# Kernel tuning notes

Measured on AMD Instinct MI355X. Metric: run time of the kernel, lower is better.

The kernel has to match this reference:

```python
import jax, jax.numpy as jnp
import numpy as np

EPS = 1e-5
NEG_SLOPE = 0.1
K = 3
KK = K * K
PAD = 1


def conv3x3(x, w, b):
    # x: [B,C,H,W], w: [O,C,3,3], zero padding 1, stride 1
    y = jax.lax.conv_general_dilated(x, w, (1, 1), [(PAD, PAD), (PAD, PAD)],
                                     dimension_numbers=('NCHW', 'OIHW', 'NCHW'))
    return y + b[None, :, None, None]


def deform_conv(x, off_w, off_b, mod_w, mod_b, w):
    # modulated deformable conv v2 (torchvision.ops.deform_conv2d semantics)
    B, C, H, W = x.shape
    offset = conv3x3(x, off_w, off_b)                      # [B,2*KK,H,W]
    mask = 2.0 * jax.nn.sigmoid(conv3x3(x, mod_w, mod_b))  # [B,KK,H,W]
    off = offset.reshape(B, KK, 2, H, W)                   # (dy,dx) per kernel pos

    ky = (jnp.arange(KK) // K).astype(x.dtype)  # kernel row of tap k
    kx = (jnp.arange(KK) % K).astype(x.dtype)   # kernel col of tap k
    hh = jnp.arange(H, dtype=x.dtype)
    ww = jnp.arange(W, dtype=x.dtype)

    # sampling positions: [B,KK,H,W]
    py = hh[None, None, :, None] - PAD + ky[None, :, None, None] + off[:, :, 0]
    px = ww[None, None, None, :] - PAD + kx[None, :, None, None] + off[:, :, 1]

    y0 = jnp.floor(py)
    x0 = jnp.floor(px)
    dy = py - y0
    dx = px - x0

    x_flat = x.reshape(B, C, H * W)

    def gather(yi, xi):
        # zero-padded bilinear corner gather -> [B,C,KK,H,W]
        valid = (yi >= 0) & (yi < H) & (xi >= 0) & (xi < W)
        yc = jnp.clip(yi, 0, H - 1).astype(jnp.int32)
        xc = jnp.clip(xi, 0, W - 1).astype(jnp.int32)
        idx = (yc * W + xc).reshape(B, 1, KK * H * W)
        g = jnp.take_along_axis(x_flat, jnp.broadcast_to(idx, (B, C, KK * H * W)), axis=2)
        return g.reshape(B, C, KK, H, W) * valid[:, None].astype(x.dtype)

    wy = dy[:, None]  # [B,1,KK,H,W]
    wx = dx[:, None]
    samp = (gather(y0, x0) * (1 - wy) * (1 - wx)
            + gather(y0, x0 + 1) * (1 - wy) * wx
            + gather(y0 + 1, x0) * wy * (1 - wx)
            + gather(y0 + 1, x0 + 1) * wy * wx)
    samp = samp * mask[:, None]
    # main conv as contraction over (C, KK)
    return jnp.einsum('bckhw,ock->bohw', samp, w.reshape(w.shape[0], C, KK))


def batch_norm(x, gamma, beta):
    # training-mode BatchNorm2d: stats over (B,H,W), biased variance
    mean = jnp.mean(x, axis=(0, 2, 3), keepdims=True)
    var = jnp.mean(jnp.square(x - mean), axis=(0, 2, 3), keepdims=True)
    xn = (x - mean) * jax.lax.rsqrt(var + EPS)
    return xn * gamma[None, :, None, None] + beta[None, :, None, None]


def leaky_relu(x):
    return jnp.where(x >= 0, x, NEG_SLOPE * x)


def setup_inputs() -> dict:
    key = jax.random.key(0)
    ks = jax.random.split(key, 12)
    B, C, H, W = 4, 96, 128, 128
    s = 1.0 / np.sqrt(C * KK)
    d = {
        'x': jax.random.normal(ks[0], (B, C, H, W), jnp.float32),
        'd1_off_w': jax.random.normal(ks[1], (2 * KK, C, K, K), jnp.float32) * s,
        'd1_off_b': jnp.zeros((2 * KK,), jnp.float32),
        'd1_mod_w': jax.random.normal(ks[2], (KK, C, K, K), jnp.float32) * s,
        'd1_mod_b': jnp.zeros((KK,), jnp.float32),
        'd1_w': jax.random.normal(ks[3], (C, C, K, K), jnp.float32) * s,
        'd2_off_w': jax.random.normal(ks[4], (2 * KK, C, K, K), jnp.float32) * s,
        'd2_off_b': jnp.zeros((2 * KK,), jnp.float32),
        'd2_mod_w': jax.random.normal(ks[5], (KK, C, K, K), jnp.float32) * s,
        'd2_mod_b': jnp.zeros((KK,), jnp.float32),
        'd2_w': jax.random.normal(ks[6], (C, C, K, K), jnp.float32) * s,
        'bn_g': jnp.ones((C,), jnp.float32),
        'bn_b': jnp.zeros((C,), jnp.float32),
    }
    return d


def reference(x, d1_off_w, d1_off_b, d1_mod_w, d1_mod_b, d1_w,
              d2_off_w, d2_off_b, d2_mod_w, d2_mod_b, d2_w, bn_g, bn_b):
    h = deform_conv(x, d1_off_w, d1_off_b, d1_mod_w, d1_mod_b, d1_w)
    h = leaky_relu(batch_norm(h, bn_g, bn_b))
    h = deform_conv(h, d2_off_w, d2_off_b, d2_mod_w, d2_mod_b, d2_w)
    h = batch_norm(h, bn_g, bn_b)  # same shared BN module (shared params)
    return x + h
```

## Files before the change

### kernel.cpp

```cpp
#include <hip/hip_runtime.h>
#include <math.h>

#define NB 4
#define NC 96
#define NH 128
#define NW 128
#define HWSZ (NH * NW)
#define NK 9
#define AUXC 27
#define CKK (NC * NK)
#define WC_ELEMS (32 * CKK)
#define WBS_STEP 4096
#define WBS_SHORTS (27 * WBS_STEP)
#define PIXB (NC * 2)
#define ZOFF ((unsigned int)(NB * HWSZ * PIXB))

typedef __attribute__((ext_vector_type(8))) short bf16x8;
typedef __attribute__((ext_vector_type(4))) float f32x4;

__device__ __forceinline__ unsigned int bf16r(float f) {
    unsigned int u = __float_as_uint(f);
    u += 0x7fffu + ((u >> 16) & 1u);
    return u >> 16;
}
__device__ __forceinline__ float uaf(unsigned int u) { return __uint_as_float(u); }

__device__ __forceinline__ unsigned int cvtpk(float lo, float hi) {
    unsigned int u;
    asm("v_cvt_pk_bf16_f32 %0, %1, %2" : "=v"(u) : "v"(lo), "v"(hi));
    return u;
}

__device__ __forceinline__ void gload_lds16(const void* g, void* l) {
    __builtin_amdgcn_global_load_lds(
        (const __attribute__((address_space(1))) void*)g,
        (__attribute__((address_space(3))) void*)l, 16, 0, 0);
}

__global__ __launch_bounds__(256) void prep_weights_kernel(
    const float* __restrict__ offw, const float* __restrict__ modw,
    const float* __restrict__ w,
    unsigned short* __restrict__ wc16, unsigned short* __restrict__ wbs)
{
    int idx = blockIdx.x * 256 + threadIdx.x;
    if (idx < WC_ELEMS) {
        int oc  = idx / CKK;
        int rem = idx - oc * CKK;
        int tap = rem / NC;
        int c   = rem - tap * NC;
        float v = 0.f;
        if (oc < 18)      v = offw[oc * CKK + c * NK + tap];
        else if (oc < 27) v = modw[(oc - 18) * CKK + c * NK + tap];
        wc16[idx] = (unsigned short)bf16r(v);
    }
    int j = idx - WC_ELEMS;
    if (j >= 0 && j < WBS_SHORTS) {
        int st = j >> 12;
        int r  = j & 4095;
        int oc = r / 40;
        int k2 = r - oc * 40;
        unsigned short v = 0;
        if (oc < NC && k2 < 32) {
            int tap = st / 3;
            int c   = (st - 3 * tap) * 32 + k2;
            v = (unsigned short)bf16r(w[oc * CKK + c * NK + tap]);
        }
        wbs[j] = v;
    }
}

__global__ __launch_bounds__(256) void nhwc_kernel(
    const float* __restrict__ in, unsigned short* __restrict__ o)
{
    __shared__ unsigned short tile[64][98];
    int t = threadIdx.x;
    int blk = blockIdx.x;
    int b  = blk >> 8;
    int p0 = (blk & 255) * 64;

    if (blk == 0 && t < NC) o[(size_t)NB * HWSZ * NC + t] = 0;

    const float* ib = in + (size_t)b * NC * HWSZ + p0;
#pragma unroll
    for (int r = 0; r < 12; ++r) {
        int e = (r * 256 + t) * 2;
        int c = e >> 6, px = e & 63;
        float2 v = *(const float2*)(ib + c * HWSZ + px);
        tile[px][c]     = (unsigned short)bf16r(v.x);
        tile[px + 1][c] = (unsigned short)bf16r(v.y);
    }
    __syncthreads();

    unsigned short* ob = o + ((size_t)b * HWSZ + p0) * NC;
#pragma unroll
    for (int r = 0; r < 12; ++r) {
        int e = (r * 256 + t) * 2;
        int px = e / 96, c = e - px * 96;
        ushort2 u;
        u.x = tile[px][c];
        u.y = tile[px][c + 1];
        *(ushort2*)(ob + e) = u;
    }
}

__global__ __launch_bounds__(256) void nhwcbn_kernel(
    const float* __restrict__ in, const float* __restrict__ sc,
    unsigned short* __restrict__ o)
{
    __shared__ unsigned short tile[64][98];
    int t = threadIdx.x;
    int blk = blockIdx.x;
    int b  = blk >> 8;
    int p0 = (blk & 255) * 64;

    const float* ib = in + (size_t)b * NC * HWSZ + p0;
#pragma unroll
    for (int r = 0; r < 12; ++r) {
        int e = (r * 256 + t) * 2;
        int c = e >> 6, px = e & 63;
        float scale = sc[c], shift = sc[NC + c];
        float2 v = *(const float2*)(ib + c * HWSZ + px);
        float ox = fmaf(scale, v.x, shift); ox = ox >= 0.f ? ox : 0.1f * ox;
        float oy = fmaf(scale, v.y, shift); oy = oy >= 0.f ? oy : 0.1f * oy;
        tile[px][c]     = (unsigned short)bf16r(ox);
        tile[px + 1][c] = (unsigned short)bf16r(oy);
    }
    __syncthreads();

    unsigned short* ob = o + ((size_t)b * HWSZ + p0) * NC;
#pragma unroll
    for (int r = 0; r < 12; ++r) {
        int e = (r * 256 + t) * 2;
        int px = e / 96, c = e - px * 96;
        ushort2 u;
        u.x = tile[px][c];
        u.y = tile[px][c + 1];
        *(ushort2*)(ob + e) = u;
    }
}

__global__ __launch_bounds__(512, 4) void conv27_mfma_kernel(
    const unsigned short* __restrict__ xhwc,
    const unsigned short* __restrict__ wc16,
    const float* __restrict__ offb, const float* __restrict__ modb,
    float* __restrict__ aux)
{
    __shared__ unsigned int sOff[NK][66];
    __shared__ float sRed[4][8][64];

    int t = threadIdx.x;
    int bid = blockIdx.x;
    int work = ((bid & 7) << 7) | (bid >> 3);
    int base = work * 64;
    int b = base >> 14;
    int rem0 = base & (HWSZ - 1);
    int y = rem0 >> 7;
    int x0 = rem0 & (NW - 1);

    for (int e = t; e < 576; e += 512) {
        int px = e & 63, k = e >> 6;
        int ky = k / 3, kx = k - 3 * (k / 3);
        int yy = y + ky - 1, xx = x0 + px + kx - 1;
        bool v = (yy >= 0) && (yy < NH) && (xx >= 0) && (xx < NW);
        sOff[k][px] = v ? (unsigned int)(((b << 14) + yy * NW + xx) * PIXB)
                        : ZOFF;
    }
    __syncthreads();

    f32x4 acc[2];
    acc[0] = (f32x4){0.f, 0.f, 0.f, 0.f};
    acc[1] = (f32x4){0.f, 0.f, 0.f, 0.f};

    const int lane15   = t & 15;
    const int g        = (t >> 4) & 3;
    const int wv       = t >> 6;
    const int nt       = wv & 3;
    const int ks       = wv >> 2;
    const int px_local = (nt << 4) | lane15;
    const int g8       = g << 3;
    const int l64      = t & 63;

    const int stbeg = ks ? 14 : 0;
    const int stend = ks ? 27 : 14;

    const char* pB = (const char*)xhwc;

    int st = stbeg;
    int tap = st / 3;
    int c2  = ((st - 3 * tap) * 32 + g8) * 2;
    bf16x8 bfr = *(const bf16x8*)(pB + sOff[tap][px_local] + c2);
    bf16x8 a0  = *(const bf16x8*)(wc16 + (size_t)lane15 * CKK + st * 32 + g8);
    bf16x8 a1  = *(const bf16x8*)(wc16 + (size_t)(16 + lane15) * CKK + st * 32 + g8);

    for (; st < stend; ++st) {
        int stn  = (st + 1 < stend) ? st + 1 : stbeg;
        int tapn = stn / 3;
        int c2n  = ((stn - 3 * tapn) * 32 + g8) * 2;
        bf16x8 bn  = *(const bf16x8*)(pB + sOff[tapn][px_local] + c2n);
        bf16x8 a0n = *(const bf16x8*)(wc16 + (size_t)lane15 * CKK + stn * 32 + g8);
        bf16x8 a1n = *(const bf16x8*)(wc16 + (size_t)(16 + lane15) * CKK + stn * 32 + g8);

        acc[0] = __builtin_amdgcn_mfma_f32_16x16x32_bf16(a0, bfr, acc[0], 0, 0, 0);
        acc[1] = __builtin_amdgcn_mfma_f32_16x16x32_bf16(a1, bfr, acc[1], 0, 0, 0);
        bfr = bn; a0 = a0n; a1 = a1n;
    }

    if (ks == 1) {
#pragma unroll
        for (int i = 0; i < 2; ++i)
#pragma unroll
            for (int r = 0; r < 4; ++r)
                sRed[nt][i * 4 + r][l64] = acc[i][r];
    }
    __syncthreads();
    if (ks == 0) {
        float* ap = aux + (size_t)b * AUXC * HWSZ + y * NW + x0 + px_local;
#pragma unroll
        for (int i = 0; i < 2; ++i) {
#pragma unroll
            for (int r = 0; r < 4; ++r) {
                int oc = i * 16 + g * 4 + r;
                float v = acc[i][r] + sRed[nt][i * 4 + r][l64];
                if (oc < 18) {
                    ap[oc * HWSZ] = v + offb[oc];
                } else if (oc < AUXC) {
                    float z = v + modb[oc - 18];
                    ap[oc * HWSZ] = 2.f / (1.f + __expf(-z));
                }
            }
        }
    }
}

__global__ __launch_bounds__(512, 4) void deform_mfma_kernel(
    const unsigned short* __restrict__ xhwc,
    const float* __restrict__ aux,
    const unsigned short* __restrict__ wbs,
    float* __restrict__ out)
{
    __shared__ uint4 sA[NK][NW];
    __shared__ uint2 sW[NK][NW];
    __shared__ unsigned short ws[2][WBS_STEP];

    int t = threadIdx.x;
    int bid = blockIdx.x;
    int work = ((bid & 7) << 6) | (bid >> 3);
    int b = work >> 7;
    int y = work & 127;

    const float* auxb = aux + (size_t)b * AUXC * HWSZ;

    for (int e = t; e < NK * NW; e += 512) {
        int px = e & 127;
        int k  = e >> 7;
        int idx = y * NW + px;
        float offy = auxb[(2 * k) * HWSZ + idx];
        float offx = auxb[(2 * k + 1) * HWSZ + idx];
        float m    = auxb[(18 + k) * HWSZ + idx];
        int ky = k / 3, kx = k - 3 * (k / 3);
        float py  = (float)(y - 1 + ky) + offy;
        float pxf = (float)(px - 1 + kx) + offx;
        float y0f = floorf(py), x0f = floorf(pxf);
        float dy = py - y0f, dx = pxf - x0f;
        int iy0 = (int)y0f, ix0 = (int)x0f;
        int iy1 = iy0 + 1,  ix1 = ix0 + 1;

        bool vy0 = (iy0 >= 0) && (iy0 < NH);
        bool vy1 = (iy1 >= 0) && (iy1 < NH);
        bool vx0 = (ix0 >= 0) && (ix0 < NW);
        bool vx1 = (ix1 >= 0) && (ix1 < NW);
        int cy0 = min(max(iy0, 0), NH - 1);
        int cy1 = min(max(iy1, 0), NH - 1);
        int cx0 = min(max(ix0, 0), NW - 1);
        int cx1 = min(max(ix1, 0), NW - 1);

        float g00 = (1.f - dy) * (1.f - dx) * m; if (!(vy0 && vx0)) g00 = 0.f;
        float g01 = (1.f - dy) * dx * m;         if (!(vy0 && vx1)) g01 = 0.f;
        float g10 = dy * (1.f - dx) * m;         if (!(vy1 && vx0)) g10 = 0.f;
        float g11 = dy * dx * m;                 if (!(vy1 && vx1)) g11 = 0.f;

        uint4 ua;
        ua.x = (unsigned int)(cy0 * NW + cx0) * PIXB;
        ua.y = (unsigned int)(cy0 * NW + cx1) * PIXB;
        ua.z = (unsigned int)(cy1 * NW + cx0) * PIXB;
        ua.w = (unsigned int)(cy1 * NW + cx1) * PIXB;
        uint2 uw;
        uw.x = bf16r(g00) | (bf16r(g01) << 16);
        uw.y = bf16r(g10) | (bf16r(g11) << 16);
        sA[k][px] = ua;
        sW[k][px] = uw;
    }

    gload_lds16((const char*)wbs + (size_t)t * 16, (char*)&ws[0][0] + t * 16);
    __syncthreads();

    f32x4 acc[6];
#pragma unroll
    for (int i = 0; i < 6; ++i) acc[i] = (f32x4){0.f, 0.f, 0.f, 0.f};

    const int lane15   = t & 15;
    const int g        = (t >> 4) & 3;
    const int wv       = t >> 6;
    const int px_local = (wv << 4) | lane15;
    const int g8       = g << 3;

    const char* pB = (const char*)(xhwc + (size_t)b * HWSZ * NC);

    uint4 ga = sA[0][px_local];
    uint2 gw = sW[0][px_local];
    bf16x8 v0 = *(const bf16x8*)(pB + ga.x + (g8 << 1));
    bf16x8 v1 = *(const bf16x8*)(pB + ga.y + (g8 << 1));
    bf16x8 v2 = *(const bf16x8*)(pB + ga.z + (g8 << 1));
    bf16x8 v3 = *(const bf16x8*)(pB + ga.w + (g8 << 1));

    int buf = 0;
    for (int st = 0; st < 27; ++st) {
        bool more = (st + 1 < 27);
        uint4 gaN; uint2 gwN;
        bf16x8 n0, n1, n2, n3;
        if (more) {
            gload_lds16((const char*)wbs + (size_t)(st + 1) * (WBS_STEP * 2) + t * 16,
                        (char*)&ws[buf ^ 1][0] + t * 16);
            int kn  = (st + 1) / 3;
            int c2n = ((st + 1 - 3 * kn) * 32 + g8) * 2;
            gaN = sA[kn][px_local];
            gwN = sW[kn][px_local];
            n0 = *(const bf16x8*)(pB + gaN.x + c2n);
            n1 = *(const bf16x8*)(pB + gaN.y + c2n);
            n2 = *(const bf16x8*)(pB + gaN.z + c2n);
            n3 = *(const bf16x8*)(pB + gaN.w + c2n);
        }

        bf16x8 afr[6];
#pragma unroll
        for (int i = 0; i < 6; ++i)
            afr[i] = *(const bf16x8*)(&ws[buf][(i * 16 + lane15) * 40 + g8]);

        float w00 = uaf(gw.x << 16), w01 = uaf(gw.x & 0xffff0000u);
        float w10 = uaf(gw.y << 16), w11 = uaf(gw.y & 0xffff0000u);
        float s[8];
#pragma unroll
        for (int j = 0; j < 8; ++j) {
            float f0 = uaf((unsigned int)(unsigned short)v0[j] << 16);
            float f1 = uaf((unsigned int)(unsigned short)v1[j] << 16);
            float f2 = uaf((unsigned int)(unsigned short)v2[j] << 16);
            float f3 = uaf((unsigned int)(unsigned short)v3[j] << 16);
            float sv = f0 * w00;
            sv = fmaf(f1, w01, sv);
            sv = fmaf(f2, w10, sv);
            sv = fmaf(f3, w11, sv);
            s[j] = sv;
        }
        union { bf16x8 h; unsigned int u[4]; } uu;
#pragma unroll
        for (int jj = 0; jj < 4; ++jj)
            uu.u[jj] = cvtpk(s[2 * jj], s[2 * jj + 1]);
        bf16x8 bfr = uu.h;

#pragma unroll
        for (int i = 0; i < 6; ++i)
            acc[i] = __builtin_amdgcn_mfma_f32_16x16x32_bf16(afr[i], bfr, acc[i], 0, 0, 0);

        if (more) {
            __syncthreads();
            ga = gaN; gw = gwN; v0 = n0; v1 = n1; v2 = n2; v3 = n3;
            buf ^= 1;
        }
    }

    float* ob = out + (size_t)b * NC * HWSZ + y * NW + px_local;
#pragma unroll
    for (int i = 0; i < 6; ++i) {
        int row0 = i * 16 + g * 4;
#pragma unroll
        for (int r = 0; r < 4; ++r)
            ob[(row0 + r) * HWSZ] = acc[i][r];
    }
}

__global__ __launch_bounds__(256) void bnstats_kernel(
    const float* __restrict__ h, float* __restrict__ part)
{
    int bc = blockIdx.x;
    const float4* p = (const float4*)(h + (size_t)bc * HWSZ);
    float s = 0.f, s2 = 0.f;
    for (int i = threadIdx.x; i < HWSZ / 4; i += 256) {
        float4 v = p[i];
        s  += v.x + v.y + v.z + v.w;
        s2 += v.x * v.x + v.y * v.y + v.z * v.z + v.w * v.w;
    }
#pragma unroll
    for (int o = 32; o > 0; o >>= 1) {
        s  += __shfl_down(s, o);
        s2 += __shfl_down(s2, o);
    }
    __shared__ float red[8];
    int wv = threadIdx.x >> 6, ln = threadIdx.x & 63;
    if (ln == 0) { red[wv] = s; red[4 + wv] = s2; }
    __syncthreads();
    if (threadIdx.x == 0) {
        part[bc]            = red[0] + red[1] + red[2] + red[3];
        part[NB * NC + bc]  = red[4] + red[5] + red[6] + red[7];
    }
}

__global__ __launch_bounds__(128) void bnfinalize_kernel(
    const float* __restrict__ part, const float* __restrict__ g,
    const float* __restrict__ bt, float* __restrict__ sc)
{
    int c = threadIdx.x;
    if (c >= NC) return;
    float s = 0.f, s2 = 0.f;
#pragma unroll
    for (int b = 0; b < NB; ++b) {
        s  += part[b * NC + c];
        s2 += part[NB * NC + b * NC + c];
    }
    const float inv_n = 1.f / (float)(NB * HWSZ);
    float mean = s * inv_n;
    float var  = s2 * inv_n - mean * mean;
    float scale = g[c] * rsqrtf(var + 1e-5f);
    sc[c] = scale;
    sc[NC + c] = bt[c] - mean * scale;
}

__global__ __launch_bounds__(256) void final_kernel(
    float* __restrict__ out, const float* __restrict__ x,
    const float* __restrict__ sc)
{
    const int n4 = NB * NC * HWSZ / 4;
    for (int i = blockIdx.x * 256 + threadIdx.x; i < n4; i += gridDim.x * 256) {
        int c = (i >> 12) % NC;
        float scale = sc[c], shift = sc[NC + c];
        float4 v = ((const float4*)out)[i];
        float4 xv = ((const float4*)x)[i];
        float4 o;
        o.x = xv.x + fmaf(scale, v.x, shift);
        o.y = xv.y + fmaf(scale, v.y, shift);
        o.z = xv.z + fmaf(scale, v.z, shift);
        o.w = xv.w + fmaf(scale, v.w, shift);
        ((float4*)out)[i] = o;
    }
}

extern "C" void kernel_launch(void* const* d_in, const int* in_sizes, int n_in,
                              void* d_out, int out_size, void* d_ws, size_t ws_size,
                              hipStream_t stream)
{
    const float* x        = (const float*)d_in[0];
    const float* d1_off_w = (const float*)d_in[1];
    const float* d1_off_b = (const float*)d_in[2];
    const float* d1_mod_w = (const float*)d_in[3];
    const float* d1_mod_b = (const float*)d_in[4];
    const float* d1_w     = (const float*)d_in[5];
    const float* d2_off_w = (const float*)d_in[6];
    const float* d2_off_b = (const float*)d_in[7];
    const float* d2_mod_w = (const float*)d_in[8];
    const float* d2_mod_b = (const float*)d_in[9];
    const float* d2_w     = (const float*)d_in[10];
    const float* bn_g     = (const float*)d_in[11];
    const float* bn_b     = (const float*)d_in[12];
    float* out = (float*)d_out;

    const size_t nImg = (size_t)NB * NC * HWSZ;
    float* h1   = (float*)d_ws;
    float* aux  = h1   + nImg;
    unsigned short* wc16 = (unsigned short*)(aux + (size_t)NB * AUXC * HWSZ);
    unsigned short* wbs  = wc16 + WC_ELEMS;
    float* sc   = (float*)(wbs + WBS_SHORTS);
    float* part = sc + 2 * NC;
    unsigned short* xhwc = (unsigned short*)(part + 2 * NB * NC);

    const int npix = NB * HWSZ;
    const int prep_blocks = (WC_ELEMS + WBS_SHORTS + 255) / 256;

    prep_weights_kernel<<<prep_blocks, 256, 0, stream>>>(d1_off_w, d1_mod_w, d1_w, wc16, wbs);
    nhwc_kernel<<<npix / 64, 256, 0, stream>>>(x, xhwc);
    conv27_mfma_kernel<<<npix / 64, 512, 0, stream>>>(xhwc, wc16, d1_off_b, d1_mod_b, aux);
    deform_mfma_kernel<<<NB * NH, 512, 0, stream>>>(xhwc, aux, wbs, h1);
    bnstats_kernel<<<NB * NC, 256, 0, stream>>>(h1, part);
    bnfinalize_kernel<<<1, 128, 0, stream>>>(part, bn_g, bn_b, sc);

    prep_weights_kernel<<<prep_blocks, 256, 0, stream>>>(d2_off_w, d2_mod_w, d2_w, wc16, wbs);
    nhwcbn_kernel<<<npix / 64, 256, 0, stream>>>(h1, sc, xhwc);
    conv27_mfma_kernel<<<npix / 64, 512, 0, stream>>>(xhwc, wc16, d2_off_b, d2_mod_b, aux);
    deform_mfma_kernel<<<NB * NH, 512, 0, stream>>>(xhwc, aux, wbs, out);
    bnstats_kernel<<<NB * NC, 256, 0, stream>>>(out, part);
    bnfinalize_kernel<<<1, 128, 0, stream>>>(part, bn_g, bn_b, sc);
    final_kernel<<<2048, 256, 0, stream>>>(out, x, sc);
}
```

Baseline: 182.0 us.

## Retile deform conv to 64-pixel blocks with deeper weight pipelining and packed indices

The deformable conv kernel now handles 64 pixels per 256-thread block instead of a 128-pixel row per 512-thread block, giving twice as many smaller blocks. Weight slices drop their 40-short padded row stride for an unpadded 32 stride, and four LDS buffers are used. The main loop is unrolled by two, prefetching two weight stages at a time and issuing the next sample's gathers before computing the current one, so there is one barrier per two stages. Corner pixel indices are packed as 16-bit pairs to halve LDS index storage. The unpadded stride may add LDS bank conflicts on the A-fragment reads.

```diff
diff --git a/kernel.cpp b/kernel.cpp
--- a/kernel.cpp
+++ b/kernel.cpp
@@ -10,7 +10,7 @@
 #define AUXC 27
 #define CKK (NC * NK)
 #define WC_ELEMS (32 * CKK)
-#define WBS_STEP 4096
+#define WBS_STEP 3072
 #define WBS_SHORTS (27 * WBS_STEP)
 #define PIXB (NC * 2)
 #define ZOFF ((unsigned int)(NB * HWSZ * PIXB))
@@ -55,17 +55,13 @@
     }
     int j = idx - WC_ELEMS;
     if (j >= 0 && j < WBS_SHORTS) {
-        int st = j >> 12;
-        int r  = j & 4095;
-        int oc = r / 40;
-        int k2 = r - oc * 40;
-        unsigned short v = 0;
-        if (oc < NC && k2 < 32) {
-            int tap = st / 3;
-            int c   = (st - 3 * tap) * 32 + k2;
-            v = (unsigned short)bf16r(w[oc * CKK + c * NK + tap]);
-        }
-        wbs[j] = v;
+        int st = j / WBS_STEP;
+        int r  = j - st * WBS_STEP;
+        int oc = r >> 5;
+        int k2 = r & 31;
+        int tap = st / 3;
+        int c   = (st - 3 * tap) * 32 + k2;
+        wbs[j] = (unsigned short)bf16r(w[oc * CKK + c * NK + tap]);
     }
 }
 
@@ -232,34 +228,40 @@
     }
 }
 
-__global__ __launch_bounds__(512, 4) void deform_mfma_kernel(
+struct Smp { uint2 gw; bf16x8 v0, v1, v2, v3; };
+
+__global__ __launch_bounds__(256, 4) void deform_mfma_kernel(
     const unsigned short* __restrict__ xhwc,
     const float* __restrict__ aux,
     const unsigned short* __restrict__ wbs,
     float* __restrict__ out)
 {
-    __shared__ uint4 sA[NK][NW];
-    __shared__ uint2 sW[NK][NW];
-    __shared__ unsigned short ws[2][WBS_STEP];
+    __shared__ uint2 sA[NK][64];
+    __shared__ uint2 sW[NK][64];
+    __shared__ unsigned short ws[4][WBS_STEP];
 
     int t = threadIdx.x;
     int bid = blockIdx.x;
-    int work = ((bid & 7) << 6) | (bid >> 3);
-    int b = work >> 7;
-    int y = work & 127;
+    int work = ((bid & 7) << 7) | (bid >> 3);
+    int base = work * 64;
+    int b = base >> 14;
+    int rem0 = base & (HWSZ - 1);
+    int y = rem0 >> 7;
+    int x0 = rem0 & (NW - 1);
 
     const float* auxb = aux + (size_t)b * AUXC * HWSZ;
 
-    for (int e = t; e < NK * NW; e += 512) {
-        int px = e & 127;
-        int k  = e >> 7;
-        int idx = y * NW + px;
+    for (int e = t; e < 576; e += 256) {
+        int px = e & 63;
+        int k  = e >> 6;
+        int xcol = x0 + px;
+        int idx = y * NW + xcol;
         float offy = auxb[(2 * k) * HWSZ + idx];
         float offx = auxb[(2 * k + 1) * HWSZ + idx];
         float m    = auxb[(18 + k) * HWSZ + idx];
         int ky = k / 3, kx = k - 3 * (k / 3);
         float py  = (float)(y - 1 + ky) + offy;
-        float pxf = (float)(px - 1 + kx) + offx;
+        float pxf = (float)(xcol - 1 + kx) + offx;
         float y0f = floorf(py), x0f = floorf(pxf);
         float dy = py - y0f, dx = pxf - x0f;
         int iy0 = (int)y0f, ix0 = (int)x0f;
@@ -279,11 +281,9 @@
         float g10 = dy * (1.f - dx) * m;         if (!(vy1 && vx0)) g10 = 0.f;
         float g11 = dy * dx * m;                 if (!(vy1 && vx1)) g11 = 0.f;
 
-        uint4 ua;
-        ua.x = (unsigned int)(cy0 * NW + cx0) * PIXB;
-        ua.y = (unsigned int)(cy0 * NW + cx1) * PIXB;
-        ua.z = (unsigned int)(cy1 * NW + cx0) * PIXB;
-        ua.w = (unsigned int)(cy1 * NW + cx1) * PIXB;
+        uint2 ua;
+        ua.x = (unsigned int)(cy0 * NW + cx0) | ((unsigned int)(cy0 * NW + cx1) << 16);
+        ua.y = (unsigned int)(cy1 * NW + cx0) | ((unsigned int)(cy1 * NW + cx1) << 16);
         uint2 uw;
         uw.x = bf16r(g00) | (bf16r(g01) << 16);
         uw.y = bf16r(g10) | (bf16r(g11) << 16);
@@ -291,13 +291,6 @@
         sW[k][px] = uw;
     }
 
-    gload_lds16((const char*)wbs + (size_t)t * 16, (char*)&ws[0][0] + t * 16);
-    __syncthreads();
-
-    f32x4 acc[6];
-#pragma unroll
-    for (int i = 0; i < 6; ++i) acc[i] = (f32x4){0.f, 0.f, 0.f, 0.f};
-
     const int lane15   = t & 15;
     const int g        = (t >> 4) & 3;
     const int wv       = t >> 6;
@@ -306,45 +299,49 @@
 
     const char* pB = (const char*)(xhwc + (size_t)b * HWSZ * NC);
 
-    uint4 ga = sA[0][px_local];
-    uint2 gw = sW[0][px_local];
-    bf16x8 v0 = *(const bf16x8*)(pB + ga.x + (g8 << 1));
-    bf16x8 v1 = *(const bf16x8*)(pB + ga.y + (g8 << 1));
-    bf16x8 v2 = *(const bf16x8*)(pB + ga.z + (g8 << 1));
-    bf16x8 v3 = *(const bf16x8*)(pB + ga.w + (g8 << 1));
-
-    int buf = 0;
-    for (int st = 0; st < 27; ++st) {
-        bool more = (st + 1 < 27);
-        uint4 gaN; uint2 gwN;
-        bf16x8 n0, n1, n2, n3;
-        if (more) {
-            gload_lds16((const char*)wbs + (size_t)(st + 1) * (WBS_STEP * 2) + t * 16,
-                        (char*)&ws[buf ^ 1][0] + t * 16);
-            int kn  = (st + 1) / 3;
-            int c2n = ((st + 1 - 3 * kn) * 32 + g8) * 2;
-            gaN = sA[kn][px_local];
-            gwN = sW[kn][px_local];
-            n0 = *(const bf16x8*)(pB + gaN.x + c2n);
-            n1 = *(const bf16x8*)(pB + gaN.y + c2n);
-            n2 = *(const bf16x8*)(pB + gaN.z + c2n);
-            n3 = *(const bf16x8*)(pB + gaN.w + c2n);
-        }
-
+    auto stage = [&](int s) {
+        const char* gp = (const char*)wbs + (size_t)s * (WBS_STEP * 2);
+        char* lp = (char*)&ws[s & 3][0];
+        gload_lds16(gp + t * 16, lp + t * 16);
+        if (t < 128)
+            gload_lds16(gp + 4096 + t * 16, lp + 4096 + t * 16);
+    };
+
+    auto loadSmp = [&](int st) -> Smp {
+        int tap = st / 3;
+        int c2  = ((st - 3 * tap) * 32 + g8) * 2;
+        uint2 ga = sA[tap][px_local];
+        Smp s;
+        s.gw = sW[tap][px_local];
+        unsigned a0 = (ga.x & 0xffffu) * PIXB + c2;
+        unsigned a1 = (ga.x >> 16) * PIXB + c2;
+        unsigned a2 = (ga.y & 0xffffu) * PIXB + c2;
+        unsigned a3 = (ga.y >> 16) * PIXB + c2;
+        s.v0 = *(const bf16x8*)(pB + a0);
+        s.v1 = *(const bf16x8*)(pB + a1);
+        s.v2 = *(const bf16x8*)(pB + a2);
+        s.v3 = *(const bf16x8*)(pB + a3);
+        return s;
+    };
+
+    f32x4 acc[6];
+#pragma unroll
+    for (int i = 0; i < 6; ++i) acc[i] = (f32x4){0.f, 0.f, 0.f, 0.f};
+
+    auto compute = [&](const Smp& sm, int buf) {
         bf16x8 afr[6];
 #pragma unroll
         for (int i = 0; i < 6; ++i)
-            afr[i] = *(const bf16x8*)(&ws[buf][(i * 16 + lane15) * 40 + g8]);
-
-        float w00 = uaf(gw.x << 16), w01 = uaf(gw.x & 0xffff0000u);
-        float w10 = uaf(gw.y << 16), w11 = uaf(gw.y & 0xffff0000u);
+            afr[i] = *(const bf16x8*)(&ws[buf][(i * 16 + lane15) * 32 + g8]);
+        float w00 = uaf(sm.gw.x << 16), w01 = uaf(sm.gw.x & 0xffff0000u);
+        float w10 = uaf(sm.gw.y << 16), w11 = uaf(sm.gw.y & 0xffff0000u);
         float s[8];
 #pragma unroll
         for (int j = 0; j < 8; ++j) {
-            float f0 = uaf((unsigned int)(unsigned short)v0[j] << 16);
-            float f1 = uaf((unsigned int)(unsigned short)v1[j] << 16);
-            float f2 = uaf((unsigned int)(unsigned short)v2[j] << 16);
-            float f3 = uaf((unsigned int)(unsigned short)v3[j] << 16);
+            float f0 = uaf((unsigned int)(unsigned short)sm.v0[j] << 16);
+            float f1 = uaf((unsigned int)(unsigned short)sm.v1[j] << 16);
+            float f2 = uaf((unsigned int)(unsigned short)sm.v2[j] << 16);
+            float f3 = uaf((unsigned int)(unsigned short)sm.v3[j] << 16);
             float sv = f0 * w00;
             sv = fmaf(f1, w01, sv);
             sv = fmaf(f2, w10, sv);
@@ -355,20 +352,29 @@
 #pragma unroll
         for (int jj = 0; jj < 4; ++jj)
             uu.u[jj] = cvtpk(s[2 * jj], s[2 * jj + 1]);
-        bf16x8 bfr = uu.h;
-
 #pragma unroll
         for (int i = 0; i < 6; ++i)
-            acc[i] = __builtin_amdgcn_mfma_f32_16x16x32_bf16(afr[i], bfr, acc[i], 0, 0, 0);
-
-        if (more) {
-            __syncthreads();
-            ga = gaN; gw = gwN; v0 = n0; v1 = n1; v2 = n2; v3 = n3;
-            buf ^= 1;
-        }
-    }
-
-    float* ob = out + (size_t)b * NC * HWSZ + y * NW + px_local;
+            acc[i] = __builtin_amdgcn_mfma_f32_16x16x32_bf16(afr[i], uu.h, acc[i], 0, 0, 0);
+    };
+
+    stage(0);
+    stage(1);
+    __syncthreads();
+
+    Smp s0 = loadSmp(0);
+    for (int st2 = 0; st2 < 26; st2 += 2) {
+        if (st2 + 2 < 27) stage(st2 + 2);
+        if (st2 + 3 < 27) stage(st2 + 3);
+        Smp s1 = loadSmp(st2 + 1);
+        compute(s0, st2 & 3);
+        Smp s2 = loadSmp(st2 + 2);
+        compute(s1, (st2 + 1) & 3);
+        __syncthreads();
+        s0 = s2;
+    }
+    compute(s0, 26 & 3);
+
+    float* ob = out + (size_t)b * NC * HWSZ + y * NW + x0 + px_local;
 #pragma unroll
     for (int i = 0; i < 6; ++i) {
         int row0 = i * 16 + g * 4;
@@ -477,14 +483,14 @@
     prep_weights_kernel<<<prep_blocks, 256, 0, stream>>>(d1_off_w, d1_mod_w, d1_w, wc16, wbs);
     nhwc_kernel<<<npix / 64, 256, 0, stream>>>(x, xhwc);
     conv27_mfma_kernel<<<npix / 64, 512, 0, stream>>>(xhwc, wc16, d1_off_b, d1_mod_b, aux);
-    deform_mfma_kernel<<<NB * NH, 512, 0, stream>>>(xhwc, aux, wbs, h1);
+    deform_mfma_kernel<<<npix / 64, 256, 0, stream>>>(xhwc, aux, wbs, h1);
     bnstats_kernel<<<NB * NC, 256, 0, stream>>>(h1, part);
     bnfinalize_kernel<<<1, 128, 0, stream>>>(part, bn_g, bn_b, sc);
 
     prep_weights_kernel<<<prep_blocks, 256, 0, stream>>>(d2_off_w, d2_mod_w, d2_w, wc16, wbs);
     nhwcbn_kernel<<<npix / 64, 256, 0, stream>>>(h1, sc, xhwc);
     conv27_mfma_kernel<<<npix / 64, 512, 0, stream>>>(xhwc, wc16, d2_off_b, d2_mod_b, aux);
-    deform_mfma_kernel<<<NB * NH, 512, 0, stream>>>(xhwc, aux, wbs, out);
+    deform_mfma_kernel<<<npix / 64, 256, 0, stream>>>(xhwc, aux, wbs, out);
     bnstats_kernel<<<NB * NC, 256, 0, stream>>>(out, part);
     bnfinalize_kernel<<<1, 128, 0, stream>>>(part, bn_g, bn_b, sc);
     final_kernel<<<2048, 256, 0, stream>>>(out, x, sc);
```

Measured after the change: 185.7 us. 2.0% more time.

## Stage offset/modulator conv weights into LDS via async double-buffered loads

Applied to the files above, without the earlier changes.

Repacks the 27-channel offset/modulator weights into per-k-step padded slabs of 32 rows by 40 shorts. The conv27 kernel now streams each slab into double-buffered shared memory with global_load_lds, replacing per-thread global reads of the A fragments. The padded row stride is meant to avoid LDS bank conflicts and cut redundant global traffic for the weights. In exchange the loop gains a __syncthreads per k-step, the kernel uses more LDS, and both K-halves must run in lockstep.

```diff
diff --git a/kernel.cpp b/kernel.cpp
--- a/kernel.cpp
+++ b/kernel.cpp
@@ -9,7 +9,8 @@
 #define NK 9
 #define AUXC 27
 #define CKK (NC * NK)
-#define WC_ELEMS (32 * CKK)
+#define WCS_STEP 1280
+#define WCS_SHORTS (27 * WCS_STEP)
 #define WBS_STEP 4096
 #define WBS_SHORTS (27 * WBS_STEP)
 #define PIXB (NC * 2)
@@ -40,20 +41,24 @@
 __global__ __launch_bounds__(256) void prep_weights_kernel(
     const float* __restrict__ offw, const float* __restrict__ modw,
     const float* __restrict__ w,
-    unsigned short* __restrict__ wc16, unsigned short* __restrict__ wbs)
+    unsigned short* __restrict__ wcs, unsigned short* __restrict__ wbs)
 {
     int idx = blockIdx.x * 256 + threadIdx.x;
-    if (idx < WC_ELEMS) {
-        int oc  = idx / CKK;
-        int rem = idx - oc * CKK;
-        int tap = rem / NC;
-        int c   = rem - tap * NC;
-        float v = 0.f;
-        if (oc < 18)      v = offw[oc * CKK + c * NK + tap];
-        else if (oc < 27) v = modw[(oc - 18) * CKK + c * NK + tap];
-        wc16[idx] = (unsigned short)bf16r(v);
-    }
-    int j = idx - WC_ELEMS;
+    if (idx < WCS_SHORTS) {
+        int st = idx / WCS_STEP;
+        int r  = idx - st * WCS_STEP;
+        int oc = r / 40;
+        int k2 = r - oc * 40;
+        unsigned short v = 0;
+        if (k2 < 32) {
+            int tap = st / 3;
+            int c   = (st - 3 * tap) * 32 + k2;
+            if (oc < 18)      v = (unsigned short)bf16r(offw[oc * CKK + c * NK + tap]);
+            else if (oc < 27) v = (unsigned short)bf16r(modw[(oc - 18) * CKK + c * NK + tap]);
+        }
+        wcs[idx] = v;
+    }
+    int j = idx - WCS_SHORTS;
     if (j >= 0 && j < WBS_SHORTS) {
         int st = j >> 12;
         int r  = j & 4095;
@@ -141,12 +146,13 @@
 
 __global__ __launch_bounds__(512, 4) void conv27_mfma_kernel(
     const unsigned short* __restrict__ xhwc,
-    const unsigned short* __restrict__ wc16,
+    const unsigned short* __restrict__ wcs,
     const float* __restrict__ offb, const float* __restrict__ modb,
     float* __restrict__ aux)
 {
     __shared__ unsigned int sOff[NK][66];
     __shared__ float sRed[4][8][64];
+    __shared__ unsigned short wr[2][2][WCS_STEP];
 
     int t = threadIdx.x;
     int bid = blockIdx.x;
@@ -157,20 +163,6 @@
     int y = rem0 >> 7;
     int x0 = rem0 & (NW - 1);
 
-    for (int e = t; e < 576; e += 512) {
-        int px = e & 63, k = e >> 6;
-        int ky = k / 3, kx = k - 3 * (k / 3);
-        int yy = y + ky - 1, xx = x0 + px + kx - 1;
-        bool v = (yy >= 0) && (yy < NH) && (xx >= 0) && (xx < NW);
-        sOff[k][px] = v ? (unsigned int)(((b << 14) + yy * NW + xx) * PIXB)
-                        : ZOFF;
-    }
-    __syncthreads();
-
-    f32x4 acc[2];
-    acc[0] = (f32x4){0.f, 0.f, 0.f, 0.f};
-    acc[1] = (f32x4){0.f, 0.f, 0.f, 0.f};
-
     const int lane15   = t & 15;
     const int g        = (t >> 4) & 3;
     const int wv       = t >> 6;
@@ -180,29 +172,56 @@
     const int g8       = g << 3;
     const int l64      = t & 63;
 
+    auto stageC = [&](int st0, int st1, int slot) {
+        if (st0 >= 0 && t < 160)
+            gload_lds16((const char*)wcs + (size_t)st0 * (WCS_STEP * 2) + t * 16,
+                        (char*)&wr[0][slot][0] + t * 16);
+        if (st1 >= 0 && t >= 256 && t < 416)
+            gload_lds16((const char*)wcs + (size_t)st1 * (WCS_STEP * 2) + (t - 256) * 16,
+                        (char*)&wr[1][slot][0] + (t - 256) * 16);
+    };
+
+    stageC(0, 14, 0);
+
+    for (int e = t; e < 576; e += 512) {
+        int px = e & 63, k = e >> 6;
+        int ky = k / 3, kx = k - 3 * (k / 3);
+        int yy = y + ky - 1, xx = x0 + px + kx - 1;
+        bool v = (yy >= 0) && (yy < NH) && (xx >= 0) && (xx < NW);
+        sOff[k][px] = v ? (unsigned int)(((b << 14) + yy * NW + xx) * PIXB)
+                        : ZOFF;
+    }
+    __syncthreads();
+
+    const char* pB = (const char*)xhwc;
+    auto loadB = [&](int st) -> bf16x8 {
+        int tap = st / 3;
+        int c2  = ((st - 3 * tap) * 32 + g8) * 2;
+        return *(const bf16x8*)(pB + sOff[tap][px_local] + c2);
+    };
+
+    f32x4 acc[2];
+    acc[0] = (f32x4){0.f, 0.f, 0.f, 0.f};
+    acc[1] = (f32x4){0.f, 0.f, 0.f, 0.f};
+
     const int stbeg = ks ? 14 : 0;
     const int stend = ks ? 27 : 14;
 
-    const char* pB = (const char*)xhwc;
-
-    int st = stbeg;
-    int tap = st / 3;
-    int c2  = ((st - 3 * tap) * 32 + g8) * 2;
-    bf16x8 bfr = *(const bf16x8*)(pB + sOff[tap][px_local] + c2);
-    bf16x8 a0  = *(const bf16x8*)(wc16 + (size_t)lane15 * CKK + st * 32 + g8);
-    bf16x8 a1  = *(const bf16x8*)(wc16 + (size_t)(16 + lane15) * CKK + st * 32 + g8);
-
-    for (; st < stend; ++st) {
-        int stn  = (st + 1 < stend) ? st + 1 : stbeg;
-        int tapn = stn / 3;
-        int c2n  = ((stn - 3 * tapn) * 32 + g8) * 2;
-        bf16x8 bn  = *(const bf16x8*)(pB + sOff[tapn][px_local] + c2n);
-        bf16x8 a0n = *(const bf16x8*)(wc16 + (size_t)lane15 * CKK + stn * 32 + g8);
-        bf16x8 a1n = *(const bf16x8*)(wc16 + (size_t)(16 + lane15) * CKK + stn * 32 + g8);
-
-        acc[0] = __builtin_amdgcn_mfma_f32_16x16x32_bf16(a0, bfr, acc[0], 0, 0, 0);
-        acc[1] = __builtin_amdgcn_mfma_f32_16x16x32_bf16(a1, bfr, acc[1], 0, 0, 0);
-        bfr = bn; a0 = a0n; a1 = a1n;
+    bf16x8 bfr = loadB(stbeg);
+
+    for (int i = 0; i < 14; ++i) {
+        int stc = stbeg + i;
+        stageC((i + 1 < 14) ? i + 1 : -1,
+               (15 + i < 27) ? 15 + i : -1, (i + 1) & 1);
+        bf16x8 bn = (stc + 1 < stend) ? loadB(stc + 1) : bfr;
+        if (stc < stend) {
+            bf16x8 a0 = *(const bf16x8*)(&wr[ks][i & 1][lane15 * 40 + g8]);
+            bf16x8 a1 = *(const bf16x8*)(&wr[ks][i & 1][(16 + lane15) * 40 + g8]);
+            acc[0] = __builtin_amdgcn_mfma_f32_16x16x32_bf16(a0, bfr, acc[0], 0, 0, 0);
+            acc[1] = __builtin_amdgcn_mfma_f32_16x16x32_bf16(a1, bfr, acc[1], 0, 0, 0);
+        }
+        __syncthreads();
+        bfr = bn;
     }
 
     if (ks == 1) {
@@ -465,25 +484,25 @@
     const size_t nImg = (size_t)NB * NC * HWSZ;
     float* h1   = (float*)d_ws;
     float* aux  = h1   + nImg;
-    unsigned short* wc16 = (unsigned short*)(aux + (size_t)NB * AUXC * HWSZ);
-    unsigned short* wbs  = wc16 + WC_ELEMS;
+    unsigned short* wcs = (unsigned short*)(aux + (size_t)NB * AUXC * HWSZ);
+    unsigned short* wbs = wcs + WCS_SHORTS;
     float* sc   = (float*)(wbs + WBS_SHORTS);
     float* part = sc + 2 * NC;
     unsigned short* xhwc = (unsigned short*)(part + 2 * NB * NC);
 
     const int npix = NB * HWSZ;
-    const int prep_blocks = (WC_ELEMS + WBS_SHORTS + 255) / 256;
-
-    prep_weights_kernel<<<prep_blocks, 256, 0, stream>>>(d1_off_w, d1_mod_w, d1_w, wc16, wbs);
+    const int prep_blocks = (WCS_SHORTS + WBS_SHORTS + 255) / 256;
+
+    prep_weights_kernel<<<prep_blocks, 256, 0, stream>>>(d1_off_w, d1_mod_w, d1_w, wcs, wbs);
     nhwc_kernel<<<npix / 64, 256, 0, stream>>>(x, xhwc);
-    conv27_mfma_kernel<<<npix / 64, 512, 0, stream>>>(xhwc, wc16, d1_off_b, d1_mod_b, aux);
+    conv27_mfma_kernel<<<npix / 64, 512, 0, stream>>>(xhwc, wcs, d1_off_b, d1_mod_b, aux);
     deform_mfma_kernel<<<NB * NH, 512, 0, stream>>>(xhwc, aux, wbs, h1);
     bnstats_kernel<<<NB * NC, 256, 0, stream>>>(h1, part);
     bnfinalize_kernel<<<1, 128, 0, stream>>>(part, bn_g, bn_b, sc);
 
-    prep_weights_kernel<<<prep_blocks, 256, 0, stream>>>(d2_off_w, d2_mod_w, d2_w, wc16, wbs);
+    prep_weights_kernel<<<prep_blocks, 256, 0, stream>>>(d2_off_w, d2_mod_w, d2_w, wcs, wbs);
     nhwcbn_kernel<<<npix / 64, 256, 0, stream>>>(h1, sc, xhwc);
-    conv27_mfma_kernel<<<npix / 64, 512, 0, stream>>>(xhwc, wc16, d2_off_b, d2_mod_b, aux);
+    conv27_mfma_kernel<<<npix / 64, 512, 0, stream>>>(xhwc, wcs, d2_off_b, d2_mod_b, aux);
     deform_mfma_kernel<<<NB * NH, 512, 0, stream>>>(xhwc, aux, wbs, out);
     bnstats_kernel<<<NB * NC, 256, 0, stream>>>(out, part);
     bnfinalize_kernel<<<1, 128, 0, stream>>>(part, bn_g, bn_b, sc);
```

New measurement: 164.4 us (median of 2 runs). -9.7%, faster.

## Fuse offset/mask conv into deformable conv kernel via shared-memory aux tile

Applied to the files above, without the earlier changes.

Merges the 27-channel offset/modulation convolution into the deformable-conv kernel. Each block computes offsets and masks for its row with MFMA and keeps them in shared memory rather than writing them to a global aux buffer and reading them back. This removes one launch per layer and the aux round trip through global memory. In exchange the conv work is no longer split across two k-halves, each wave now runs all 27 steps serially without software prefetch, and the block needs more shared memory, which may lower occupancy.

```diff
diff --git a/kernel.cpp b/kernel.cpp
--- a/kernel.cpp
+++ b/kernel.cpp
@@ -139,108 +139,17 @@
     }
 }
 
-__global__ __launch_bounds__(512, 4) void conv27_mfma_kernel(
+__global__ __launch_bounds__(512, 4) void fused_layer_kernel(
     const unsigned short* __restrict__ xhwc,
     const unsigned short* __restrict__ wc16,
+    const unsigned short* __restrict__ wbs,
     const float* __restrict__ offb, const float* __restrict__ modb,
-    float* __restrict__ aux)
-{
-    __shared__ unsigned int sOff[NK][66];
-    __shared__ float sRed[4][8][64];
-
-    int t = threadIdx.x;
-    int bid = blockIdx.x;
-    int work = ((bid & 7) << 7) | (bid >> 3);
-    int base = work * 64;
-    int b = base >> 14;
-    int rem0 = base & (HWSZ - 1);
-    int y = rem0 >> 7;
-    int x0 = rem0 & (NW - 1);
-
-    for (int e = t; e < 576; e += 512) {
-        int px = e & 63, k = e >> 6;
-        int ky = k / 3, kx = k - 3 * (k / 3);
-        int yy = y + ky - 1, xx = x0 + px + kx - 1;
-        bool v = (yy >= 0) && (yy < NH) && (xx >= 0) && (xx < NW);
-        sOff[k][px] = v ? (unsigned int)(((b << 14) + yy * NW + xx) * PIXB)
-                        : ZOFF;
-    }
-    __syncthreads();
-
-    f32x4 acc[2];
-    acc[0] = (f32x4){0.f, 0.f, 0.f, 0.f};
-    acc[1] = (f32x4){0.f, 0.f, 0.f, 0.f};
-
-    const int lane15   = t & 15;
-    const int g        = (t >> 4) & 3;
-    const int wv       = t >> 6;
-    const int nt       = wv & 3;
-    const int ks       = wv >> 2;
-    const int px_local = (nt << 4) | lane15;
-    const int g8       = g << 3;
-    const int l64      = t & 63;
-
-    const int stbeg = ks ? 14 : 0;
-    const int stend = ks ? 27 : 14;
-
-    const char* pB = (const char*)xhwc;
-
-    int st = stbeg;
-    int tap = st / 3;
-    int c2  = ((st - 3 * tap) * 32 + g8) * 2;
-    bf16x8 bfr = *(const bf16x8*)(pB + sOff[tap][px_local] + c2);
-    bf16x8 a0  = *(const bf16x8*)(wc16 + (size_t)lane15 * CKK + st * 32 + g8);
-    bf16x8 a1  = *(const bf16x8*)(wc16 + (size_t)(16 + lane15) * CKK + st * 32 + g8);
-
-    for (; st < stend; ++st) {
-        int stn  = (st + 1 < stend) ? st + 1 : stbeg;
-        int tapn = stn / 3;
-        int c2n  = ((stn - 3 * tapn) * 32 + g8) * 2;
-        bf16x8 bn  = *(const bf16x8*)(pB + sOff[tapn][px_local] + c2n);
-        bf16x8 a0n = *(const bf16x8*)(wc16 + (size_t)lane15 * CKK + stn * 32 + g8);
-        bf16x8 a1n = *(const bf16x8*)(wc16 + (size_t)(16 + lane15) * CKK + stn * 32 + g8);
-
-        acc[0] = __builtin_amdgcn_mfma_f32_16x16x32_bf16(a0, bfr, acc[0], 0, 0, 0);
-        acc[1] = __builtin_amdgcn_mfma_f32_16x16x32_bf16(a1, bfr, acc[1], 0, 0, 0);
-        bfr = bn; a0 = a0n; a1 = a1n;
-    }
-
-    if (ks == 1) {
-#pragma unroll
-        for (int i = 0; i < 2; ++i)
-#pragma unroll
-            for (int r = 0; r < 4; ++r)
-                sRed[nt][i * 4 + r][l64] = acc[i][r];
-    }
-    __syncthreads();
-    if (ks == 0) {
-        float* ap = aux + (size_t)b * AUXC * HWSZ + y * NW + x0 + px_local;
-#pragma unroll
-        for (int i = 0; i < 2; ++i) {
-#pragma unroll
-            for (int r = 0; r < 4; ++r) {
-                int oc = i * 16 + g * 4 + r;
-                float v = acc[i][r] + sRed[nt][i * 4 + r][l64];
-                if (oc < 18) {
-                    ap[oc * HWSZ] = v + offb[oc];
-                } else if (oc < AUXC) {
-                    float z = v + modb[oc - 18];
-                    ap[oc * HWSZ] = 2.f / (1.f + __expf(-z));
-                }
-            }
-        }
-    }
-}
-
-__global__ __launch_bounds__(512, 4) void deform_mfma_kernel(
-    const unsigned short* __restrict__ xhwc,
-    const float* __restrict__ aux,
-    const unsigned short* __restrict__ wbs,
     float* __restrict__ out)
 {
     __shared__ uint4 sA[NK][NW];
     __shared__ uint2 sW[NK][NW];
     __shared__ unsigned short ws[2][WBS_STEP];
+    __shared__ float auxT[AUXC][NW + 1];
 
     int t = threadIdx.x;
     int bid = blockIdx.x;
@@ -248,15 +157,60 @@
     int b = work >> 7;
     int y = work & 127;
 
-    const float* auxb = aux + (size_t)b * AUXC * HWSZ;
+    const int lane15   = t & 15;
+    const int g        = (t >> 4) & 3;
+    const int wv       = t >> 6;
+    const int px_local = (wv << 4) | lane15;
+    const int g8       = g << 3;
+
+    const char* pB = (const char*)xhwc;
+
+    gload_lds16((const char*)wbs + (size_t)t * 16, (char*)&ws[0][0] + t * 16);
+
+    {
+        f32x4 cacc[2];
+        cacc[0] = (f32x4){0.f, 0.f, 0.f, 0.f};
+        cacc[1] = (f32x4){0.f, 0.f, 0.f, 0.f};
+
+#pragma unroll 3
+        for (int st = 0; st < 27; ++st) {
+            int tap = st / 3;
+            int c2  = ((st - 3 * tap) * 32 + g8) * 2;
+            int ky = tap / 3, kx = tap - 3 * ky;
+            int yy = y + ky - 1, xx = px_local + kx - 1;
+            bool v = (yy >= 0) && (yy < NH) && (xx >= 0) && (xx < NW);
+            unsigned int boff = v ? (unsigned int)(((b << 14) + yy * NW + xx) * PIXB)
+                                  : ZOFF;
+            bf16x8 bfr = *(const bf16x8*)(pB + boff + c2);
+            bf16x8 a0 = *(const bf16x8*)(wc16 + (size_t)lane15 * CKK + st * 32 + g8);
+            bf16x8 a1 = *(const bf16x8*)(wc16 + (size_t)(16 + lane15) * CKK + st * 32 + g8);
+            cacc[0] = __builtin_amdgcn_mfma_f32_16x16x32_bf16(a0, bfr, cacc[0], 0, 0, 0);
+            cacc[1] = __builtin_amdgcn_mfma_f32_16x16x32_bf16(a1, bfr, cacc[1], 0, 0, 0);
+        }
+
+#pragma unroll
+        for (int i = 0; i < 2; ++i) {
+#pragma unroll
+            for (int r = 0; r < 4; ++r) {
+                int oc = i * 16 + g * 4 + r;
+                float v = cacc[i][r];
+                if (oc < 18) {
+                    auxT[oc][px_local] = v + offb[oc];
+                } else if (oc < AUXC) {
+                    float z = v + modb[oc - 18];
+                    auxT[oc][px_local] = 2.f / (1.f + __expf(-z));
+                }
+            }
+        }
+    }
+    __syncthreads();
 
     for (int e = t; e < NK * NW; e += 512) {
         int px = e & 127;
         int k  = e >> 7;
-        int idx = y * NW + px;
-        float offy = auxb[(2 * k) * HWSZ + idx];
-        float offx = auxb[(2 * k + 1) * HWSZ + idx];
-        float m    = auxb[(18 + k) * HWSZ + idx];
+        float offy = auxT[2 * k][px];
+        float offx = auxT[2 * k + 1][px];
+        float m    = auxT[18 + k][px];
         int ky = k / 3, kx = k - 3 * (k / 3);
         float py  = (float)(y - 1 + ky) + offy;
         float pxf = (float)(px - 1 + kx) + offx;
@@ -290,28 +244,20 @@
         sA[k][px] = ua;
         sW[k][px] = uw;
     }
-
-    gload_lds16((const char*)wbs + (size_t)t * 16, (char*)&ws[0][0] + t * 16);
     __syncthreads();
 
     f32x4 acc[6];
 #pragma unroll
     for (int i = 0; i < 6; ++i) acc[i] = (f32x4){0.f, 0.f, 0.f, 0.f};
 
-    const int lane15   = t & 15;
-    const int g        = (t >> 4) & 3;
-    const int wv       = t >> 6;
-    const int px_local = (wv << 4) | lane15;
-    const int g8       = g << 3;
-
-    const char* pB = (const char*)(xhwc + (size_t)b * HWSZ * NC);
+    const char* pBb = (const char*)(xhwc + (size_t)b * HWSZ * NC);
 
     uint4 ga = sA[0][px_local];
     uint2 gw = sW[0][px_local];
-    bf16x8 v0 = *(const bf16x8*)(pB + ga.x + (g8 << 1));
-    bf16x8 v1 = *(const bf16x8*)(pB + ga.y + (g8 << 1));
-    bf16x8 v2 = *(const bf16x8*)(pB + ga.z + (g8 << 1));
-    bf16x8 v3 = *(const bf16x8*)(pB + ga.w + (g8 << 1));
+    bf16x8 v0 = *(const bf16x8*)(pBb + ga.x + (g8 << 1));
+    bf16x8 v1 = *(const bf16x8*)(pBb + ga.y + (g8 << 1));
+    bf16x8 v2 = *(const bf16x8*)(pBb + ga.z + (g8 << 1));
+    bf16x8 v3 = *(const bf16x8*)(pBb + ga.w + (g8 << 1));
 
     int buf = 0;
     for (int st = 0; st < 27; ++st) {
@@ -325,10 +271,10 @@
             int c2n = ((st + 1 - 3 * kn) * 32 + g8) * 2;
             gaN = sA[kn][px_local];
             gwN = sW[kn][px_local];
-            n0 = *(const bf16x8*)(pB + gaN.x + c2n);
-            n1 = *(const bf16x8*)(pB + gaN.y + c2n);
-            n2 = *(const bf16x8*)(pB + gaN.z + c2n);
-            n3 = *(const bf16x8*)(pB + gaN.w + c2n);
+            n0 = *(const bf16x8*)(pBb + gaN.x + c2n);
+            n1 = *(const bf16x8*)(pBb + gaN.y + c2n);
+            n2 = *(const bf16x8*)(pBb + gaN.z + c2n);
+            n3 = *(const bf16x8*)(pBb + gaN.w + c2n);
         }
 
         bf16x8 afr[6];
@@ -464,8 +410,7 @@
 
     const size_t nImg = (size_t)NB * NC * HWSZ;
     float* h1   = (float*)d_ws;
-    float* aux  = h1   + nImg;
-    unsigned short* wc16 = (unsigned short*)(aux + (size_t)NB * AUXC * HWSZ);
+    unsigned short* wc16 = (unsigned short*)(h1 + nImg);
     unsigned short* wbs  = wc16 + WC_ELEMS;
     float* sc   = (float*)(wbs + WBS_SHORTS);
     float* part = sc + 2 * NC;
@@ -476,15 +421,13 @@
 
     prep_weights_kernel<<<prep_blocks, 256, 0, stream>>>(d1_off_w, d1_mod_w, d1_w, wc16, wbs);
     nhwc_kernel<<<npix / 64, 256, 0, stream>>>(x, xhwc);
-    conv27_mfma_kernel<<<npix / 64, 512, 0, stream>>>(xhwc, wc16, d1_off_b, d1_mod_b, aux);
-    deform_mfma_kernel<<<NB * NH, 512, 0, stream>>>(xhwc, aux, wbs, h1);
+    fused_layer_kernel<<<NB * NH, 512, 0, stream>>>(xhwc, wc16, wbs, d1_off_b, d1_mod_b, h1);
     bnstats_kernel<<<NB * NC, 256, 0, stream>>>(h1, part);
     bnfinalize_kernel<<<1, 128, 0, stream>>>(part, bn_g, bn_b, sc);
 
     prep_weights_kernel<<<prep_blocks, 256, 0, stream>>>(d2_off_w, d2_mod_w, d2_w, wc16, wbs);
     nhwcbn_kernel<<<npix / 64, 256, 0, stream>>>(h1, sc, xhwc);
-    conv27_mfma_kernel<<<npix / 64, 512, 0, stream>>>(xhwc, wc16, d2_off_b, d2_mod_b, aux);
-    deform_mfma_kernel<<<NB * NH, 512, 0, stream>>>(xhwc, aux, wbs, out);
+    fused_layer_kernel<<<NB * NH, 512, 0, stream>>>(xhwc, wc16, wbs, d2_off_b, d2_mod_b, out);
     bnstats_kernel<<<NB * NC, 256, 0, stream>>>(out, part);
     bnfinalize_kernel<<<1, 128, 0, stream>>>(part, bn_g, bn_b, sc);
     final_kernel<<<2048, 256, 0, stream>>>(out, x, sc);
```

New measurement: 178.4 us. -2.0%, faster.
